# Optimization experiments

Measured on AMD Instinct MI355X. Metric: run time of the kernel, lower is better.

Reference implementation:

```python
import jax, jax.numpy as jnp
import numpy as np

C_RADIUS = 20.0  # weighted-L1 ball radius from the cvxpy constraint
EPS = 1e-30


def weighted_l1_ball_projection(q, w, c):
    """Euclidean projection of each row of q onto {x : sum_i w_i*|x_i| <= c}, w>=0.
    Closed-form via sorted breakpoints: x_i = sign(q_i)*max(|q_i| - lam*w_i, 0).
    q, w: [B, D].
    """
    aq = jnp.abs(q)
    wa = w * aq                               # w_i |q_i|
    feasible = jnp.sum(wa, axis=-1) <= c      # already inside the ball
    # breakpoint ratios; coords with w==0 are never clipped -> push to the end
    r = jnp.where(w > 0, aq / jnp.maximum(w, EPS), -jnp.inf)
    order = jnp.argsort(-r, axis=-1)
    wa_s = jnp.take_along_axis(wa, order, axis=-1)
    w2_s = jnp.take_along_axis(w * w, order, axis=-1)
    r_s = jnp.take_along_axis(r, order, axis=-1)
    A = jnp.cumsum(wa_s, axis=-1)             # prefix sums over candidate active sets
    B = jnp.cumsum(w2_s, axis=-1)
    lam_k = (A - c) / jnp.maximum(B, EPS)
    valid = r_s > lam_k                       # active-set condition
    k = jnp.sum(valid, axis=-1)               # size of true active set
    idx = jnp.maximum(k - 1, 0)
    lam = jnp.take_along_axis(lam_k, idx[:, None], axis=-1)[:, 0]
    lam = jnp.where(feasible, 0.0, jnp.maximum(lam, 0.0))
    return jnp.sign(q) * jnp.maximum(aq - lam[:, None] * w, 0.0)


def setup_inputs() -> dict:
    key = jax.random.key(0)
    ks = jax.random.split(key, 8)
    state_dim, action_dim, B = 17, 6, 262144
    # scale state so the weighted-L1 constraint is occasionally active
    state = 4.0 * jax.random.normal(ks[0], (B, state_dim), dtype=jnp.float32)
    def lin(kw, kb, fan_out, fan_in):
        bound = 1.0 / np.sqrt(fan_in)
        W = jax.random.uniform(kw, (fan_out, fan_in), jnp.float32, -bound, bound)
        b = jax.random.uniform(kb, (fan_out,), jnp.float32, -bound, bound)
        return W, b
    l1_w, l1_b = lin(ks[1], ks[2], 400, state_dim)
    l2_w, l2_b = lin(ks[3], ks[4], 300, 400)
    l3_w, l3_b = lin(ks[5], ks[6], action_dim, 300)
    return {"state": state, "l1_w": l1_w, "l1_b": l1_b, "l2_w": l2_w,
            "l2_b": l2_b, "l3_w": l3_w, "l3_b": l3_b, "training": 0}


def reference(state, l1_w, l1_b, l2_w, l2_b, l3_w, l3_b, training):
    max_action = 1.0
    a = jax.nn.relu(state @ l1_w.T + l1_b)
    a = jax.nn.relu(a @ l2_w.T + l2_b)
    scaled_a = max_action * jnp.tanh(a @ l3_w.T + l3_b)  # [B, 6]
    # IS_TRAINING path: QP  min 0.5||x||^2 - q^T x  s.t. sum |x_i * s[11+i]| <= 20
    w = jnp.abs(state[:, 11:17])
    return weighted_l1_ball_projection(scaled_a, w, C_RADIUS)
```

## Files before the change

### kernel.cpp

```cpp
#include <hip/hip_runtime.h>
#include <math.h>

typedef _Float16 half8 __attribute__((ext_vector_type(8)));
typedef float floatx4 __attribute__((ext_vector_type(4)));

#define C_RADIUS 20.0f


__global__ void actor_prep(const float* __restrict__ w1, const float* __restrict__ b1,
                           const float* __restrict__ w2, const float* __restrict__ b2,
                           const float* __restrict__ w3, const float* __restrict__ b3,
                           _Float16* __restrict__ ws) {
  int gid = blockIdx.x * 256 + threadIdx.x;
  if (gid >= 19072) return;
  half8 hv;
  _Float16* dst;
  if (gid < 1792) {
    int l = gid & 63, tn = gid >> 6;
    int n = tn * 16 + (l & 15);
    int kc = 8 * (l >> 4);
#pragma unroll
    for (int e = 0; e < 8; ++e) {
      int k = kc + e;
      float v = 0.f;
      if (n < 400) {
        if (k < 17) v = w1[n * 17 + k];
        else if (k == 17) v = b1[n];
      }
      hv[e] = (_Float16)v;
    }
    dst = ws + gid * 8;
  } else if (gid < 1792 + 16640) {
    int g = gid - 1792;
    int l = g & 63, t = g >> 6;
    int ks = t % 13, tn = t / 13;
    int n = tn * 16 + (l & 15);
    int kc = ks * 32 + 8 * (l >> 4);
#pragma unroll
    for (int e = 0; e < 8; ++e) {
      int k = kc + e;
      float v = 0.f;
      if (n < 300) {
        if (k < 400) v = w2[n * 400 + k];
        else if (k == 400) v = b2[n];
      }
      hv[e] = (_Float16)v;
    }
    dst = ws + 14336 + g * 8;
  } else {
    int g = gid - 1792 - 16640;
    int l = g & 63, ks = g >> 6;
    int n = l & 15;
    int kc = ks * 32 + 8 * (l >> 4);
#pragma unroll
    for (int e = 0; e < 8; ++e) {
      int k = kc + e;
      float v = 0.f;
      if (n < 6) {
        if (k < 300) v = w3[n * 300 + k];
        else if (k == 300) v = b3[n];
      }
      hv[e] = (_Float16)v;
    }
    dst = ws + 147456 + g * 8;
  }
  *reinterpret_cast<half8*>(dst) = hv;
}

static __device__ __forceinline__ int a_slot(int ks, int row, int ch) {
  return (ks * 64 + row) * 4 + (ch ^ ((row >> 1) & 3));
}

__global__ __launch_bounds__(512, 4) void actor_fused(const float* __restrict__ state,
                                                      const _Float16* __restrict__ ws,
                                                      float* __restrict__ out) {
  __shared__ __align__(16) _Float16 aL[13 * 64 * 32];
  __shared__ float stateL[64 * 18];
  __shared__ float z3L[64 * 8];
  __shared__ __align__(16) float outL[64 * 6];

  const int tid = threadIdx.x;
  const int lane = tid & 63;
  const int w = tid >> 6;
  const int r15 = lane & 15;
  const int c4 = lane >> 4;
  const int row0 = blockIdx.x * 64;

  for (int i = tid; i < 64 * 17; i += 512) {
    int r = i / 17;
    int c = i - r * 17;
    stateL[r * 18 + c] = state[row0 * 17 + i];
  }
  for (int i = tid; i < 2048; i += 512) {
    int row = i >> 5;
    int j = i & 31;
    int j0 = (2 ^ ((row >> 1) & 3)) * 8;
    aL[12 * 64 * 32 + i] = (j == j0) ? (_Float16)1.0f : (_Float16)0.0f;
  }
  __syncthreads();

  {
    half8 aF[4];
#pragma unroll
    for (int m = 0; m < 4; ++m) {
      half8 v;
#pragma unroll
      for (int e = 0; e < 8; ++e) {
        int k = 8 * c4 + e;
        float x = 0.f;
        if (k < 17) x = stateL[(16 * m + r15) * 18 + k];
        else if (k == 17) x = 1.0f;
        v[e] = (_Float16)x;
      }
      aF[m] = v;
    }
    const half8* W1f = reinterpret_cast<const half8*>(ws);
#pragma unroll
    for (int t = 0; t < 4; ++t) {
      int tn = w + 8 * t;
      if (tn < 25) {
        half8 bF = W1f[tn * 64 + lane];
        floatx4 acc[4];
#pragma unroll
        for (int m = 0; m < 4; ++m)
          acc[m] = __builtin_amdgcn_mfma_f32_16x16x32_f16(aF[m], bF, (floatx4){0.f, 0.f, 0.f, 0.f}, 0, 0, 0);
        int col = tn * 16 + r15;
        int ks = col >> 5, ch = (col >> 3) & 3, e = col & 7;
#pragma unroll
        for (int m = 0; m < 4; ++m)
#pragma unroll
          for (int r = 0; r < 4; ++r) {
            int row = 16 * m + 4 * c4 + r;
            float v = acc[m][r];
            v = v > 0.f ? v : 0.f;
            aL[a_slot(ks, row, ch) * 8 + e] = (_Float16)v;
          }
      }
    }
  }
  __syncthreads();

  {
    const half8* W2f = reinterpret_cast<const half8*>(ws + 14336);
    const int nt = (w < 4) ? 3 : 2;
    const int tn0 = (w < 4) ? (w * 3) : (12 + (w - 4) * 2);
    floatx4 acc[4][3];
#pragma unroll
    for (int m = 0; m < 4; ++m)
#pragma unroll
      for (int t = 0; t < 3; ++t) acc[m][t] = (floatx4){0.f, 0.f, 0.f, 0.f};

    half8 bF[3], bFn[3];
#pragma unroll
    for (int t = 0; t < 3; ++t)
      if (t < nt) bF[t] = W2f[((tn0 + t) * 13 + 0) * 64 + lane];

#pragma unroll 1
    for (int ks = 0; ks < 13; ++ks) {
      if (ks + 1 < 13) {
#pragma unroll
        for (int t = 0; t < 3; ++t)
          if (t < nt) bFn[t] = W2f[((tn0 + t) * 13 + ks + 1) * 64 + lane];
      }
      half8 aF[4];
#pragma unroll
      for (int m = 0; m < 4; ++m)
        aF[m] = *reinterpret_cast<const half8*>(&aL[a_slot(ks, 16 * m + r15, c4) * 8]);
#pragma unroll
      for (int t = 0; t < 3; ++t)
        if (t < nt)
#pragma unroll
          for (int m = 0; m < 4; ++m)
            acc[m][t] = __builtin_amdgcn_mfma_f32_16x16x32_f16(aF[m], bF[t], acc[m][t], 0, 0, 0);
#pragma unroll
      for (int t = 0; t < 3; ++t) bF[t] = bFn[t];
    }
    __syncthreads();

#pragma unroll
    for (int t = 0; t < 3; ++t)
      if (t < nt) {
        int col = (tn0 + t) * 16 + r15;
        int ks2 = col >> 5, ch = (col >> 3) & 3, e = col & 7;
#pragma unroll
        for (int m = 0; m < 4; ++m)
#pragma unroll
          for (int r = 0; r < 4; ++r) {
            int row = 16 * m + 4 * c4 + r;
            float v = acc[m][t][r];
            v = v > 0.f ? v : 0.f;
            if (col == 300) v = 1.0f;
            aL[a_slot(ks2, row, ch) * 8 + e] = (_Float16)v;
          }
      }
  }
  __syncthreads();

  if (w < 4) {
    const half8* W3f = reinterpret_cast<const half8*>(ws + 147456);
    floatx4 accA = (floatx4){0.f, 0.f, 0.f, 0.f};
    floatx4 accB = (floatx4){0.f, 0.f, 0.f, 0.f};
    int row = 16 * w + r15;
#pragma unroll
    for (int ks = 0; ks < 10; ks += 2) {
      half8 f0 = *reinterpret_cast<const half8*>(&aL[a_slot(ks, row, c4) * 8]);
      half8 f1 = *reinterpret_cast<const half8*>(&aL[a_slot(ks + 1, row, c4) * 8]);
      accA = __builtin_amdgcn_mfma_f32_16x16x32_f16(f0, W3f[ks * 64 + lane], accA, 0, 0, 0);
      accB = __builtin_amdgcn_mfma_f32_16x16x32_f16(f1, W3f[(ks + 1) * 64 + lane], accB, 0, 0, 0);
    }
    floatx4 z = accA + accB;
    if (r15 < 6) {
#pragma unroll
      for (int r = 0; r < 4; ++r) {
        int orow = 16 * w + 4 * c4 + r;
        z3L[orow * 8 + r15] = tanhf(z[r]);
      }
    }
  }
  __syncthreads();

  if (tid < 64) {
    const int row = tid;
    float q[6], wv[6], aq[6], wa[6];
    float S = 0.f;
#pragma unroll
    for (int i = 0; i < 6; ++i) {
      q[i] = z3L[row * 8 + i];
      wv[i] = fabsf(stateL[row * 18 + 11 + i]);
      aq[i] = fabsf(q[i]);
      wa[i] = wv[i] * aq[i];
      S += wa[i];
    }
    float lam = 0.f;
    if (!(S <= C_RADIUS)) {
      float rr[6], w2s[6], was[6];
#pragma unroll
      for (int i = 0; i < 6; ++i) {
        rr[i] = (wv[i] > 0.f) ? (aq[i] / fmaxf(wv[i], 1e-30f)) : -__builtin_inff();
        w2s[i] = wv[i] * wv[i];
        was[i] = wa[i];
      }
#pragma unroll
      for (int p = 0; p < 5; ++p)
#pragma unroll
        for (int j2 = 0; j2 < 5; ++j2)
          if (j2 < 5 - p) {
            if (rr[j2] < rr[j2 + 1]) {
              float t0 = rr[j2];  rr[j2] = rr[j2 + 1];  rr[j2 + 1] = t0;
              float t1 = w2s[j2]; w2s[j2] = w2s[j2 + 1]; w2s[j2 + 1] = t1;
              float t2 = was[j2]; was[j2] = was[j2 + 1]; was[j2 + 1] = t2;
            }
          }
      float A = 0.f, Bc = 0.f;
      float lamk[6];
      int kc = 0;
#pragma unroll
      for (int i = 0; i < 6; ++i) {
        A += was[i];
        Bc += w2s[i];
        lamk[i] = (A - C_RADIUS) / fmaxf(Bc, 1e-30f);
        if (rr[i] > lamk[i]) ++kc;
      }
      int idx = kc - 1;
      if (idx < 0) idx = 0;
      float lsel = lamk[0];
#pragma unroll
      for (int i = 1; i < 6; ++i)
        if (i == idx) lsel = lamk[i];
      lam = fmaxf(lsel, 0.f);
    }
#pragma unroll
    for (int i = 0; i < 6; ++i) {
      float x = fmaxf(aq[i] - lam * wv[i], 0.f);
      outL[row * 6 + i] = copysignf(x, q[i]);
    }
  }
  __syncthreads();

  if (tid < 96) {
    float4 v = reinterpret_cast<const float4*>(outL)[tid];
    reinterpret_cast<float4*>(out)[blockIdx.x * 96 + tid] = v;
  }
}

extern "C" void kernel_launch(void* const* d_in, const int* in_sizes, int n_in,
                              void* d_out, int out_size, void* d_ws, size_t ws_size,
                              hipStream_t stream) {
  const float* state = (const float*)d_in[0];
  const float* w1 = (const float*)d_in[1];
  const float* b1 = (const float*)d_in[2];
  const float* w2 = (const float*)d_in[3];
  const float* b2 = (const float*)d_in[4];
  const float* w3 = (const float*)d_in[5];
  const float* b3 = (const float*)d_in[6];
  _Float16* ws = (_Float16*)d_ws;
  float* out = (float*)d_out;

  actor_prep<<<75, 256, 0, stream>>>(w1, b1, w2, b2, w3, b3, ws);
  actor_fused<<<4096, 512, 0, stream>>>(state, ws, out);
}
```

Measured before the change: 111.3 us.

## Use transposed LDS reads with 16x16x16 MFMA and software-pipelined A fragments

Reorders the activation and weight layouts so A fragments are fetched with ds_read_b64_tr_b16 transposed LDS reads and fed to 16x16x16 f16 MFMAs. The layer-2 loop is double-buffered with explicit lgkmcnt waits to overlap LDS reads with MFMA work. Activations are packed with cvt_pkrtz into half4 stores, and tanh is replaced with an exp-based approximation. Risks include round-toward-zero conversion and fast tanh shifting accuracy, plus hand-written waitcnt and scheduling assumptions that must hold.

```diff
diff --git a/kernel.cpp b/kernel.cpp
--- a/kernel.cpp
+++ b/kernel.cpp
@@ -1,6 +1,9 @@
 #include <hip/hip_runtime.h>
 #include <math.h>
 
+typedef _Float16 half2v __attribute__((ext_vector_type(2)));
+typedef __fp16 fp16x2 __attribute__((ext_vector_type(2)));
+typedef _Float16 half4 __attribute__((ext_vector_type(4)));
 typedef _Float16 half8 __attribute__((ext_vector_type(8)));
 typedef float floatx4 __attribute__((ext_vector_type(4)));
 
@@ -18,10 +21,9 @@
   if (gid < 1792) {
     int l = gid & 63, tn = gid >> 6;
     int n = tn * 16 + (l & 15);
-    int kc = 8 * (l >> 4);
 #pragma unroll
     for (int e = 0; e < 8; ++e) {
-      int k = kc + e;
+      int k = 16 * (e >> 2) + 4 * (l >> 4) + (e & 3);
       float v = 0.f;
       if (n < 400) {
         if (k < 17) v = w1[n * 17 + k];
@@ -35,10 +37,9 @@
     int l = g & 63, t = g >> 6;
     int ks = t % 13, tn = t / 13;
     int n = tn * 16 + (l & 15);
-    int kc = ks * 32 + 8 * (l >> 4);
 #pragma unroll
     for (int e = 0; e < 8; ++e) {
-      int k = kc + e;
+      int k = 32 * ks + 16 * (e >> 2) + 4 * (l >> 4) + (e & 3);
       float v = 0.f;
       if (n < 300) {
         if (k < 400) v = w2[n * 400 + k];
@@ -51,10 +52,9 @@
     int g = gid - 1792 - 16640;
     int l = g & 63, ks = g >> 6;
     int n = l & 15;
-    int kc = ks * 32 + 8 * (l >> 4);
 #pragma unroll
     for (int e = 0; e < 8; ++e) {
-      int k = kc + e;
+      int k = 32 * ks + 16 * (e >> 2) + 4 * (l >> 4) + (e & 3);
       float v = 0.f;
       if (n < 6) {
         if (k < 300) v = w3[n * 300 + k];
@@ -67,17 +67,49 @@
   *reinterpret_cast<half8*>(dst) = hv;
 }
 
-static __device__ __forceinline__ int a_slot(int ks, int row, int ch) {
-  return (ks * 64 + row) * 4 + (ch ^ ((row >> 1) & 3));
+
+#define TRD(dst, addr, OFF) \
+  asm volatile("ds_read_b64_tr_b16 %0, %1 offset:" OFF : "=v"(dst) : "v"(addr))
+
+#define ISSUE_A(buf, addr)                                   \
+  do {                                                       \
+    TRD(buf[0], addr, "0");    TRD(buf[1], addr, "128");     \
+    TRD(buf[2], addr, "256");  TRD(buf[3], addr, "384");     \
+    TRD(buf[4], addr, "2048"); TRD(buf[5], addr, "2176");    \
+    TRD(buf[6], addr, "2304"); TRD(buf[7], addr, "2432");    \
+  } while (0)
+
+#define LGKM(N)                                              \
+  do {                                                       \
+    asm volatile("s_waitcnt lgkmcnt(" #N ")" ::: "memory");  \
+    __builtin_amdgcn_sched_barrier(0);                       \
+  } while (0)
+
+#define LO4(x) __builtin_shufflevector(x, x, 0, 1, 2, 3)
+#define HI4(x) __builtin_shufflevector(x, x, 4, 5, 6, 7)
+#define MFMA16(A, B, C) C = __builtin_amdgcn_mfma_f32_16x16x16f16(A, B, C, 0, 0, 0)
+
+__device__ __forceinline__ half4 pack4(float v0, float v1, float v2, float v3) {
+  fp16x2 a = __builtin_amdgcn_cvt_pkrtz(v0, v1);
+  fp16x2 b = __builtin_amdgcn_cvt_pkrtz(v2, v3);
+  half2v a2 = __builtin_bit_cast(half2v, a);
+  half2v b2 = __builtin_bit_cast(half2v, b);
+  return __builtin_shufflevector(a2, b2, 0, 1, 2, 3);
+}
+
+__device__ __forceinline__ float fast_tanh(float x) {
+  float e = __expf(2.0f * x);
+  return 1.0f - 2.0f / (e + 1.0f);
 }
 
 __global__ __launch_bounds__(512, 4) void actor_fused(const float* __restrict__ state,
                                                       const _Float16* __restrict__ ws,
                                                       float* __restrict__ out) {
-  __shared__ __align__(16) _Float16 aL[13 * 64 * 32];
-  __shared__ float stateL[64 * 18];
+  __shared__ __align__(128) _Float16 aL[26624];
+  __shared__ __align__(128) _Float16 stateF[2048];
   __shared__ float z3L[64 * 8];
   __shared__ __align__(16) float outL[64 * 6];
+  __shared__ float wvL[64 * 6];
 
   const int tid = threadIdx.x;
   const int lane = tid & 63;
@@ -86,55 +118,58 @@
   const int c4 = lane >> 4;
   const int row0 = blockIdx.x * 64;
 
-  for (int i = tid; i < 64 * 17; i += 512) {
-    int r = i / 17;
-    int c = i - r * 17;
-    stateL[r * 18 + c] = state[row0 * 17 + i];
-  }
-  for (int i = tid; i < 2048; i += 512) {
-    int row = i >> 5;
-    int j = i & 31;
-    int j0 = (2 ^ ((row >> 1) & 3)) * 8;
-    aL[12 * 64 * 32 + i] = (j == j0) ? (_Float16)1.0f : (_Float16)0.0f;
+  const unsigned aBase = (unsigned)(size_t)(&aL[0]);
+  const unsigned sBase = (unsigned)(size_t)(&stateF[0]);
+
+  for (int i = tid; i < 1024; i += 512) {
+    int blk = i >> 5, q = i & 31, ci = q >> 3, s = q & 7;
+    int kb = blk >> 2, rb = blk & 3;
+    int row = rb * 16 + 2 * s, col = kb * 4 + ci;
+    float v0 = 0.f, v1 = 0.f;
+    if (col < 17) {
+      v0 = state[(row0 + row) * 17 + col];
+      v1 = state[(row0 + row + 1) * 17 + col];
+    } else if (col == 17) {
+      v0 = 1.f; v1 = 1.f;
+    }
+    half2v h = {(_Float16)v0, (_Float16)v1};
+    *reinterpret_cast<half2v*>(reinterpret_cast<char*>(stateF) + blk * 128 + ci * 32 + 4 * s) = h;
+  }
+  for (int i = tid; i < 1024; i += 512)
+    aL[25600 + i] = (i < 256 && (i & 63) < 16) ? (_Float16)1.0f : (_Float16)0.0f;
+  if (tid < 384) {
+    int r = tid / 6, c = tid - r * 6;
+    wvL[tid] = fabsf(state[(row0 + r) * 17 + 11 + c]);
   }
   __syncthreads();
 
   {
-    half8 aF[4];
-#pragma unroll
-    for (int m = 0; m < 4; ++m) {
-      half8 v;
-#pragma unroll
-      for (int e = 0; e < 8; ++e) {
-        int k = 8 * c4 + e;
-        float x = 0.f;
-        if (k < 17) x = stateL[(16 * m + r15) * 18 + k];
-        else if (k == 17) x = 1.0f;
-        v[e] = (_Float16)x;
-      }
-      aF[m] = v;
-    }
+    half4 S[8];
+    unsigned sA = sBase + c4 * 512 + r15 * 8;
+    ISSUE_A(S, sA);
+    LGKM(0);
     const half8* W1f = reinterpret_cast<const half8*>(ws);
 #pragma unroll
     for (int t = 0; t < 4; ++t) {
       int tn = w + 8 * t;
       if (tn < 25) {
-        half8 bF = W1f[tn * 64 + lane];
+        half8 bw = W1f[tn * 64 + lane];
+        half4 blo = LO4(bw), bhi = HI4(bw);
         floatx4 acc[4];
 #pragma unroll
-        for (int m = 0; m < 4; ++m)
-          acc[m] = __builtin_amdgcn_mfma_f32_16x16x32_f16(aF[m], bF, (floatx4){0.f, 0.f, 0.f, 0.f}, 0, 0, 0);
+        for (int m = 0; m < 4; ++m) {
+          acc[m] = (floatx4){0.f, 0.f, 0.f, 0.f};
+          MFMA16(S[m], blo, acc[m]);
+          MFMA16(S[4 + m], bhi, acc[m]);
+        }
         int col = tn * 16 + r15;
-        int ks = col >> 5, ch = (col >> 3) & 3, e = col & 7;
-#pragma unroll
-        for (int m = 0; m < 4; ++m)
-#pragma unroll
-          for (int r = 0; r < 4; ++r) {
-            int row = 16 * m + 4 * c4 + r;
-            float v = acc[m][r];
-            v = v > 0.f ? v : 0.f;
-            aL[a_slot(ks, row, ch) * 8 + e] = (_Float16)v;
-          }
+        int wrel = ((col >> 2) * 4) * 128 + (col & 3) * 32 + 8 * c4;
+#pragma unroll
+        for (int m = 0; m < 4; ++m) {
+          half4 hv = pack4(fmaxf(acc[m][0], 0.f), fmaxf(acc[m][1], 0.f),
+                           fmaxf(acc[m][2], 0.f), fmaxf(acc[m][3], 0.f));
+          *reinterpret_cast<half4*>(reinterpret_cast<char*>(aL) + wrel + m * 128) = hv;
+        }
       }
     }
   }
@@ -150,70 +185,110 @@
 #pragma unroll
       for (int t = 0; t < 3; ++t) acc[m][t] = (floatx4){0.f, 0.f, 0.f, 0.f};
 
-    half8 bF[3], bFn[3];
+    half4 A0[8], A1[8];
+    half8 bX[3], bY[3];
+    unsigned aE = aBase + c4 * 512 + r15 * 8;
+    unsigned aO = aE + 4096;
+
+    ISSUE_A(A0, aE);
 #pragma unroll
     for (int t = 0; t < 3; ++t)
-      if (t < nt) bF[t] = W2f[((tn0 + t) * 13 + 0) * 64 + lane];
+      if (t < nt) bX[t] = W2f[((tn0 + t) * 13 + 0) * 64 + lane];
 
 #pragma unroll 1
-    for (int ks = 0; ks < 13; ++ks) {
-      if (ks + 1 < 13) {
-#pragma unroll
-        for (int t = 0; t < 3; ++t)
-          if (t < nt) bFn[t] = W2f[((tn0 + t) * 13 + ks + 1) * 64 + lane];
-      }
-      half8 aF[4];
-#pragma unroll
-      for (int m = 0; m < 4; ++m)
-        aF[m] = *reinterpret_cast<const half8*>(&aL[a_slot(ks, 16 * m + r15, c4) * 8]);
+    for (int i = 0; i < 6; ++i) {
+      int ks1 = 2 * i + 1, ks2 = 2 * i + 2;
+      ISSUE_A(A1, aO);
+      aO += 8192;
 #pragma unroll
       for (int t = 0; t < 3; ++t)
-        if (t < nt)
-#pragma unroll
-          for (int m = 0; m < 4; ++m)
-            acc[m][t] = __builtin_amdgcn_mfma_f32_16x16x32_f16(aF[m], bF[t], acc[m][t], 0, 0, 0);
-#pragma unroll
-      for (int t = 0; t < 3; ++t) bF[t] = bFn[t];
-    }
+        if (t < nt) bY[t] = W2f[((tn0 + t) * 13 + ks1) * 64 + lane];
+      LGKM(8);
+#pragma unroll
+      for (int t = 0; t < 3; ++t)
+        if (t < nt) {
+          half4 blo = LO4(bX[t]), bhi = HI4(bX[t]);
+#pragma unroll
+          for (int m = 0; m < 4; ++m) {
+            MFMA16(A0[m], blo, acc[m][t]);
+            MFMA16(A0[4 + m], bhi, acc[m][t]);
+          }
+        }
+      aE += 8192;
+      ISSUE_A(A0, aE);
+#pragma unroll
+      for (int t = 0; t < 3; ++t)
+        if (t < nt) bX[t] = W2f[((tn0 + t) * 13 + ks2) * 64 + lane];
+      LGKM(8);
+#pragma unroll
+      for (int t = 0; t < 3; ++t)
+        if (t < nt) {
+          half4 blo = LO4(bY[t]), bhi = HI4(bY[t]);
+#pragma unroll
+          for (int m = 0; m < 4; ++m) {
+            MFMA16(A1[m], blo, acc[m][t]);
+            MFMA16(A1[4 + m], bhi, acc[m][t]);
+          }
+        }
+    }
+    LGKM(0);
+#pragma unroll
+    for (int t = 0; t < 3; ++t)
+      if (t < nt) {
+        half4 blo = LO4(bX[t]), bhi = HI4(bX[t]);
+#pragma unroll
+        for (int m = 0; m < 4; ++m) {
+          MFMA16(A0[m], blo, acc[m][t]);
+          MFMA16(A0[4 + m], bhi, acc[m][t]);
+        }
+      }
+
     __syncthreads();
 
 #pragma unroll
     for (int t = 0; t < 3; ++t)
       if (t < nt) {
         int col = (tn0 + t) * 16 + r15;
-        int ks2 = col >> 5, ch = (col >> 3) & 3, e = col & 7;
-#pragma unroll
-        for (int m = 0; m < 4; ++m)
-#pragma unroll
-          for (int r = 0; r < 4; ++r) {
-            int row = 16 * m + 4 * c4 + r;
-            float v = acc[m][t][r];
-            v = v > 0.f ? v : 0.f;
-            if (col == 300) v = 1.0f;
-            aL[a_slot(ks2, row, ch) * 8 + e] = (_Float16)v;
-          }
+        int wrel = ((col >> 2) * 4) * 128 + (col & 3) * 32 + 8 * c4;
+#pragma unroll
+        for (int m = 0; m < 4; ++m) {
+          float v0 = fmaxf(acc[m][t][0], 0.f), v1 = fmaxf(acc[m][t][1], 0.f);
+          float v2 = fmaxf(acc[m][t][2], 0.f), v3 = fmaxf(acc[m][t][3], 0.f);
+          if (col == 300) { v0 = 1.f; v1 = 1.f; v2 = 1.f; v3 = 1.f; }
+          half4 hv = pack4(v0, v1, v2, v3);
+          *reinterpret_cast<half4*>(reinterpret_cast<char*>(aL) + wrel + m * 128) = hv;
+        }
       }
   }
   __syncthreads();
 
   if (w < 4) {
     const half8* W3f = reinterpret_cast<const half8*>(ws + 147456);
-    floatx4 accA = (floatx4){0.f, 0.f, 0.f, 0.f};
-    floatx4 accB = (floatx4){0.f, 0.f, 0.f, 0.f};
-    int row = 16 * w + r15;
+    floatx4 za = (floatx4){0.f, 0.f, 0.f, 0.f};
+    floatx4 zb = (floatx4){0.f, 0.f, 0.f, 0.f};
+    unsigned a3 = aBase + w * 128 + c4 * 512 + r15 * 8;
 #pragma unroll
     for (int ks = 0; ks < 10; ks += 2) {
-      half8 f0 = *reinterpret_cast<const half8*>(&aL[a_slot(ks, row, c4) * 8]);
-      half8 f1 = *reinterpret_cast<const half8*>(&aL[a_slot(ks + 1, row, c4) * 8]);
-      accA = __builtin_amdgcn_mfma_f32_16x16x32_f16(f0, W3f[ks * 64 + lane], accA, 0, 0, 0);
-      accB = __builtin_amdgcn_mfma_f32_16x16x32_f16(f1, W3f[(ks + 1) * 64 + lane], accB, 0, 0, 0);
-    }
-    floatx4 z = accA + accB;
+      half4 f0, f1, f2, f3;
+      TRD(f0, a3, "0");
+      TRD(f1, a3, "2048");
+      TRD(f2, a3, "4096");
+      TRD(f3, a3, "6144");
+      half8 w0 = W3f[ks * 64 + lane];
+      half8 w1_ = W3f[(ks + 1) * 64 + lane];
+      LGKM(0);
+      MFMA16(f0, LO4(w0), za);
+      MFMA16(f1, HI4(w0), za);
+      MFMA16(f2, LO4(w1_), zb);
+      MFMA16(f3, HI4(w1_), zb);
+      a3 += 8192;
+    }
+    floatx4 z = za + zb;
     if (r15 < 6) {
 #pragma unroll
       for (int r = 0; r < 4; ++r) {
         int orow = 16 * w + 4 * c4 + r;
-        z3L[orow * 8 + r15] = tanhf(z[r]);
+        z3L[orow * 8 + r15] = fast_tanh(z[r]);
       }
     }
   }
@@ -226,7 +301,7 @@
 #pragma unroll
     for (int i = 0; i < 6; ++i) {
       q[i] = z3L[row * 8 + i];
-      wv[i] = fabsf(stateL[row * 18 + 11 + i]);
+      wv[i] = wvL[row * 6 + i];
       aq[i] = fabsf(q[i]);
       wa[i] = wv[i] * aq[i];
       S += wa[i];
```

After: 110.2 us. No clear change (-1.0%).

## Use padded row-major LDS activations with transposed MFMA and packed half4 stores

Applied to the files above, without the earlier changes.

Replaces the XOR-swizzled k-chunk layout for activations in shared memory with padded row-major layouts. It also swaps the MFMA operand order so each lane holds four consecutive output columns, which lets the epilogue write them as one packed half4 store instead of scattered scalar fp16 stores. The state tile is converted to fp16 with its bias column when it is loaded, the weights are cached in a separate array, and tanh becomes an exp-based fast version. The padding strides may still cause some LDS bank conflicts, and the fast tanh is slightly less accurate.

```diff
diff --git a/kernel.cpp b/kernel.cpp
--- a/kernel.cpp
+++ b/kernel.cpp
@@ -1,6 +1,9 @@
 #include <hip/hip_runtime.h>
 #include <math.h>
 
+typedef _Float16 half2v __attribute__((ext_vector_type(2)));
+typedef __fp16 fp16x2 __attribute__((ext_vector_type(2)));
+typedef _Float16 half4 __attribute__((ext_vector_type(4)));
 typedef _Float16 half8 __attribute__((ext_vector_type(8)));
 typedef float floatx4 __attribute__((ext_vector_type(4)));
 
@@ -67,17 +70,33 @@
   *reinterpret_cast<half8*>(dst) = hv;
 }
 
-static __device__ __forceinline__ int a_slot(int ks, int row, int ch) {
-  return (ks * 64 + row) * 4 + (ch ^ ((row >> 1) & 3));
+#define LD1 424
+#define LD2 328
+#define LDS_ 40
+
+#define MFMA32(A, B, C) C = __builtin_amdgcn_mfma_f32_16x16x32_f16(A, B, C, 0, 0, 0)
+
+__device__ __forceinline__ half4 pack4(float v0, float v1, float v2, float v3) {
+  fp16x2 a = __builtin_amdgcn_cvt_pkrtz(v0, v1);
+  fp16x2 b = __builtin_amdgcn_cvt_pkrtz(v2, v3);
+  half2v a2 = __builtin_bit_cast(half2v, a);
+  half2v b2 = __builtin_bit_cast(half2v, b);
+  return __builtin_shufflevector(a2, b2, 0, 1, 2, 3);
+}
+
+__device__ __forceinline__ float fast_tanh(float x) {
+  float e = __expf(2.0f * x);
+  return 1.0f - 2.0f / (e + 1.0f);
 }
 
 __global__ __launch_bounds__(512, 4) void actor_fused(const float* __restrict__ state,
                                                       const _Float16* __restrict__ ws,
                                                       float* __restrict__ out) {
-  __shared__ __align__(16) _Float16 aL[13 * 64 * 32];
-  __shared__ float stateL[64 * 18];
+  __shared__ __align__(16) _Float16 aL[64 * LD1];
+  __shared__ __align__(16) _Float16 stateF[64 * LDS_];
   __shared__ float z3L[64 * 8];
   __shared__ __align__(16) float outL[64 * 6];
+  __shared__ float wvL[64 * 6];
 
   const int tid = threadIdx.x;
   const int lane = tid & 63;
@@ -86,55 +105,48 @@
   const int c4 = lane >> 4;
   const int row0 = blockIdx.x * 64;
 
-  for (int i = tid; i < 64 * 17; i += 512) {
-    int r = i / 17;
-    int c = i - r * 17;
-    stateL[r * 18 + c] = state[row0 * 17 + i];
-  }
-  for (int i = tid; i < 2048; i += 512) {
-    int row = i >> 5;
-    int j = i & 31;
-    int j0 = (2 ^ ((row >> 1) & 3)) * 8;
-    aL[12 * 64 * 32 + i] = (j == j0) ? (_Float16)1.0f : (_Float16)0.0f;
+  for (int i = tid; i < 1088; i += 512) {
+    int r = i / 17, c = i - r * 17;
+    stateF[r * LDS_ + c] = (_Float16)state[row0 * 17 + i];
+  }
+  for (int i = tid; i < 64 * 23; i += 512) {
+    int r = i / 23, c = 17 + (i - r * 23);
+    stateF[r * LDS_ + c] = (c == 17) ? (_Float16)1.0f : (_Float16)0.0f;
+  }
+  for (int i = tid; i < 1024; i += 512) {
+    int r = i >> 4, c = i & 15;
+    aL[r * LD1 + 400 + c] = (c == 0) ? (_Float16)1.0f : (_Float16)0.0f;
+  }
+  if (tid < 384) {
+    int r = tid / 6, c = tid - r * 6;
+    wvL[tid] = fabsf(state[(row0 + r) * 17 + 11 + c]);
   }
   __syncthreads();
 
   {
-    half8 aF[4];
-#pragma unroll
-    for (int m = 0; m < 4; ++m) {
-      half8 v;
-#pragma unroll
-      for (int e = 0; e < 8; ++e) {
-        int k = 8 * c4 + e;
-        float x = 0.f;
-        if (k < 17) x = stateL[(16 * m + r15) * 18 + k];
-        else if (k == 17) x = 1.0f;
-        v[e] = (_Float16)x;
-      }
-      aF[m] = v;
-    }
+    half8 S[4];
+#pragma unroll
+    for (int m = 0; m < 4; ++m)
+      S[m] = *reinterpret_cast<const half8*>(&stateF[(16 * m + r15) * LDS_ + 8 * c4]);
     const half8* W1f = reinterpret_cast<const half8*>(ws);
 #pragma unroll
     for (int t = 0; t < 4; ++t) {
       int tn = w + 8 * t;
       if (tn < 25) {
-        half8 bF = W1f[tn * 64 + lane];
+        half8 aW = W1f[tn * 64 + lane];
         floatx4 acc[4];
 #pragma unroll
-        for (int m = 0; m < 4; ++m)
-          acc[m] = __builtin_amdgcn_mfma_f32_16x16x32_f16(aF[m], bF, (floatx4){0.f, 0.f, 0.f, 0.f}, 0, 0, 0);
-        int col = tn * 16 + r15;
-        int ks = col >> 5, ch = (col >> 3) & 3, e = col & 7;
-#pragma unroll
-        for (int m = 0; m < 4; ++m)
-#pragma unroll
-          for (int r = 0; r < 4; ++r) {
-            int row = 16 * m + 4 * c4 + r;
-            float v = acc[m][r];
-            v = v > 0.f ? v : 0.f;
-            aL[a_slot(ks, row, ch) * 8 + e] = (_Float16)v;
-          }
+        for (int m = 0; m < 4; ++m) {
+          acc[m] = (floatx4){0.f, 0.f, 0.f, 0.f};
+          MFMA32(aW, S[m], acc[m]);
+        }
+        int n0 = tn * 16 + 4 * c4;
+#pragma unroll
+        for (int m = 0; m < 4; ++m) {
+          half4 hv = pack4(fmaxf(acc[m][0], 0.f), fmaxf(acc[m][1], 0.f),
+                           fmaxf(acc[m][2], 0.f), fmaxf(acc[m][3], 0.f));
+          *reinterpret_cast<half4*>(&aL[(16 * m + r15) * LD1 + n0]) = hv;
+        }
       }
     }
   }
@@ -150,71 +162,68 @@
 #pragma unroll
       for (int t = 0; t < 3; ++t) acc[m][t] = (floatx4){0.f, 0.f, 0.f, 0.f};
 
-    half8 bF[3], bFn[3];
+    half8 bX[3], bY[3];
 #pragma unroll
     for (int t = 0; t < 3; ++t)
-      if (t < nt) bF[t] = W2f[((tn0 + t) * 13 + 0) * 64 + lane];
+      if (t < nt) bX[t] = W2f[((tn0 + t) * 13 + 0) * 64 + lane];
 
 #pragma unroll 1
     for (int ks = 0; ks < 13; ++ks) {
-      if (ks + 1 < 13) {
+      if (ks < 12) {
 #pragma unroll
         for (int t = 0; t < 3; ++t)
-          if (t < nt) bFn[t] = W2f[((tn0 + t) * 13 + ks + 1) * 64 + lane];
-      }
-      half8 aF[4];
+          if (t < nt) bY[t] = W2f[((tn0 + t) * 13 + ks + 1) * 64 + lane];
+      }
+      half8 F[4];
 #pragma unroll
       for (int m = 0; m < 4; ++m)
-        aF[m] = *reinterpret_cast<const half8*>(&aL[a_slot(ks, 16 * m + r15, c4) * 8]);
+        F[m] = *reinterpret_cast<const half8*>(&aL[(16 * m + r15) * LD1 + ks * 32 + 8 * c4]);
 #pragma unroll
       for (int t = 0; t < 3; ++t)
         if (t < nt)
 #pragma unroll
           for (int m = 0; m < 4; ++m)
-            acc[m][t] = __builtin_amdgcn_mfma_f32_16x16x32_f16(aF[m], bF[t], acc[m][t], 0, 0, 0);
-#pragma unroll
-      for (int t = 0; t < 3; ++t) bF[t] = bFn[t];
+            MFMA32(bX[t], F[m], acc[m][t]);
+#pragma unroll
+      for (int t = 0; t < 3; ++t) bX[t] = bY[t];
     }
     __syncthreads();
 
 #pragma unroll
     for (int t = 0; t < 3; ++t)
       if (t < nt) {
-        int col = (tn0 + t) * 16 + r15;
-        int ks2 = col >> 5, ch = (col >> 3) & 3, e = col & 7;
-#pragma unroll
-        for (int m = 0; m < 4; ++m)
-#pragma unroll
-          for (int r = 0; r < 4; ++r) {
-            int row = 16 * m + 4 * c4 + r;
-            float v = acc[m][t][r];
-            v = v > 0.f ? v : 0.f;
-            if (col == 300) v = 1.0f;
-            aL[a_slot(ks2, row, ch) * 8 + e] = (_Float16)v;
-          }
+        int n0 = (tn0 + t) * 16 + 4 * c4;
+#pragma unroll
+        for (int m = 0; m < 4; ++m) {
+          float v0 = fmaxf(acc[m][t][0], 0.f), v1 = fmaxf(acc[m][t][1], 0.f);
+          float v2 = fmaxf(acc[m][t][2], 0.f), v3 = fmaxf(acc[m][t][3], 0.f);
+          if (n0 == 300) v0 = 1.0f;
+          half4 hv = pack4(v0, v1, v2, v3);
+          *reinterpret_cast<half4*>(&aL[(16 * m + r15) * LD2 + n0]) = hv;
+        }
       }
   }
   __syncthreads();
 
   if (w < 4) {
     const half8* W3f = reinterpret_cast<const half8*>(ws + 147456);
-    floatx4 accA = (floatx4){0.f, 0.f, 0.f, 0.f};
-    floatx4 accB = (floatx4){0.f, 0.f, 0.f, 0.f};
-    int row = 16 * w + r15;
+    floatx4 za = (floatx4){0.f, 0.f, 0.f, 0.f};
+    floatx4 zb = (floatx4){0.f, 0.f, 0.f, 0.f};
+    const int row = 16 * w + r15;
 #pragma unroll
     for (int ks = 0; ks < 10; ks += 2) {
-      half8 f0 = *reinterpret_cast<const half8*>(&aL[a_slot(ks, row, c4) * 8]);
-      half8 f1 = *reinterpret_cast<const half8*>(&aL[a_slot(ks + 1, row, c4) * 8]);
-      accA = __builtin_amdgcn_mfma_f32_16x16x32_f16(f0, W3f[ks * 64 + lane], accA, 0, 0, 0);
-      accB = __builtin_amdgcn_mfma_f32_16x16x32_f16(f1, W3f[(ks + 1) * 64 + lane], accB, 0, 0, 0);
-    }
-    floatx4 z = accA + accB;
-    if (r15 < 6) {
-#pragma unroll
-      for (int r = 0; r < 4; ++r) {
-        int orow = 16 * w + 4 * c4 + r;
-        z3L[orow * 8 + r15] = tanhf(z[r]);
-      }
+      half8 F0 = *reinterpret_cast<const half8*>(&aL[row * LD2 + ks * 32 + 8 * c4]);
+      half8 F1 = *reinterpret_cast<const half8*>(&aL[row * LD2 + (ks + 1) * 32 + 8 * c4]);
+      MFMA32(W3f[ks * 64 + lane], F0, za);
+      MFMA32(W3f[(ks + 1) * 64 + lane], F1, zb);
+    }
+    floatx4 z = za + zb;
+    if (c4 == 0) {
+#pragma unroll
+      for (int j = 0; j < 4; ++j) z3L[row * 8 + j] = fast_tanh(z[j]);
+    } else if (c4 == 1) {
+      z3L[row * 8 + 4] = fast_tanh(z[0]);
+      z3L[row * 8 + 5] = fast_tanh(z[1]);
     }
   }
   __syncthreads();
@@ -226,7 +235,7 @@
 #pragma unroll
     for (int i = 0; i < 6; ++i) {
       q[i] = z3L[row * 8 + i];
-      wv[i] = fabsf(stateL[row * 18 + 11 + i]);
+      wv[i] = wvL[row * 6 + i];
       aq[i] = fabsf(q[i]);
       wa[i] = wv[i] * aq[i];
       S += wa[i];
```

Result: faster. 97.10 us (-12.8%).
